# Kernel tuning notes

Measured on AMD Instinct MI355X. Metric: run time of the kernel, lower is better.

## Reference

```python
import jax, jax.numpy as jnp
import numpy as np

B, N, C, H = 32, 577, 768, 12
D = C // H  # head_dim = 64


def _rotate_half(t):
    half = t.shape[-1] // 2
    return jnp.concatenate([-t[..., half:], t[..., :half]], axis=-1)


def _rope(t, sin, cos):
    # t: [B, H, N-1, D]; sin/cos: [N-1, D] broadcast over batch and heads
    return t * cos + _rotate_half(t) * sin


def setup_inputs() -> dict:
    key = jax.random.key(0)
    ks = jax.random.split(key, 5)
    x = jax.random.normal(ks[0], (B, N, C), dtype=jnp.float32)
    w_qkv = jax.random.normal(ks[1], (C, 3 * C), dtype=jnp.float32) * (1.0 / np.sqrt(C))
    b_qkv = jnp.zeros((3 * C,), dtype=jnp.float32)
    w_proj = jax.random.normal(ks[2], (C, C), dtype=jnp.float32) * (1.0 / np.sqrt(C))
    b_proj = jnp.zeros((C,), dtype=jnp.float32)
    # rotary tables for the N-1 non-CLS tokens
    pos = jnp.arange(N - 1, dtype=jnp.float32)[:, None]            # [N-1, 1]
    inv_freq = 1.0 / (10000.0 ** (jnp.arange(0, D, 2, dtype=jnp.float32) / D))  # [D/2]
    ang = pos * inv_freq[None, :]                                   # [N-1, D/2]
    ang = jnp.concatenate([ang, ang], axis=-1)                      # [N-1, D]
    rope_sin = jnp.sin(ang)
    rope_cos = jnp.cos(ang)
    return {"x": x, "w_qkv": w_qkv, "b_qkv": b_qkv, "w_proj": w_proj,
            "b_proj": b_proj, "rope_sin": rope_sin, "rope_cos": rope_cos}


def reference(x, w_qkv, b_qkv, w_proj, b_proj, rope_sin, rope_cos):
    Bx, Nx, Cx = x.shape
    qkv = x @ w_qkv + b_qkv                                   # [B, N, 3C]
    qkv = qkv.reshape(Bx, Nx, 3, H, D).transpose(2, 0, 3, 1, 4)  # [3, B, H, N, D]
    q, k, v = qkv[0], qkv[1], qkv[2]
    # RoPE only on non-CLS tokens (index 0 is CLS)
    q = jnp.concatenate([q[:, :, :1, :], _rope(q[:, :, 1:, :], rope_sin, rope_cos)], axis=2)
    k = jnp.concatenate([k[:, :, :1, :], _rope(k[:, :, 1:, :], rope_sin, rope_cos)], axis=2)
    q = q / jnp.sqrt(jnp.float32(D))
    attn = jnp.einsum("bhqd,bhkd->bhqk", q, k)               # [B, H, N, N]
    attn = jax.nn.softmax(attn.astype(jnp.float32), axis=-1).astype(x.dtype)
    out = jnp.einsum("bhqk,bhkd->bhqd", attn, v)             # [B, H, N, D]
    out = out.transpose(0, 2, 1, 3).reshape(Bx, Nx, Cx)       # [B, N, C]
    return out @ w_proj + b_proj
```

## Files before the change

kernel.cpp:

```cpp
#include <hip/hip_runtime.h>

#define Bdim 32
#define Ndim 577
#define Cdim 768
#define Hdim 12
#define Ddim 64
#define Mdim (Bdim*Ndim)
#define VSTRIDE 640
#define TSTRIDE 152
#define QSCALE 0.18033688f
#define MGRP 19

typedef __attribute__((ext_vector_type(4))) float f32x4;
typedef __attribute__((ext_vector_type(8))) __bf16 bf16x8;
typedef __attribute__((ext_vector_type(4))) __bf16 bf16x4;

__device__ __forceinline__ void gl_lds16(const __bf16* g, __bf16* l) {
  __builtin_amdgcn_global_load_lds((const __attribute__((address_space(1))) void*)g,
                                   (__attribute__((address_space(3))) void*)l, 16, 0, 0);
}

__global__ __launch_bounds__(256) void f32_to_bf16(const float4* __restrict__ in,
                                                   bf16x4* __restrict__ out, int n4) {
  int i = blockIdx.x * 256 + threadIdx.x;
  if (i < n4) {
    float4 v = in[i];
    bf16x4 o = {(__bf16)v.x, (__bf16)v.y, (__bf16)v.z, (__bf16)v.w};
    out[i] = o;
  }
}

__global__ __launch_bounds__(256) void transpose_f32_bf16(const float* __restrict__ in,
                                                          __bf16* __restrict__ out,
                                                          int R, int Cc) {
  __shared__ float tile[64][65];
  int bx = blockIdx.x * 64;
  int by = blockIdx.y * 64;
  int tx = threadIdx.x & 63, ty = threadIdx.x >> 6;
  for (int i = ty; i < 64; i += 4) {
    int r = by + i, c = bx + tx;
    tile[i][tx] = (r < R && c < Cc) ? in[(size_t)r * Cc + c] : 0.f;
  }
  __syncthreads();
  for (int i = ty; i < 64; i += 4) {
    int r = bx + i, c = by + tx;
    if (r < Cc && c < R) out[(size_t)r * R + c] = (__bf16)tile[tx][i];
  }
}

__global__ __launch_bounds__(256) void transpose_f32_wfrag(const float* __restrict__ in,
                                                           __bf16* __restrict__ out) {
  __shared__ float tile[64][65];
  int bx = blockIdx.x * 64;
  int by = blockIdx.y * 64;
  int tx = threadIdx.x & 63, ty = threadIdx.x >> 6;
  #pragma unroll
  for (int i = ty; i < 64; i += 4)
    tile[i][tx] = in[(size_t)(by + i) * 2304 + bx + tx];
  __syncthreads();
  #pragma unroll
  for (int it = 0; it < 2; ++it) {
    int idx = it * 256 + threadIdx.x;
    int nl = idx & 63, kc = idx >> 6;
    bf16x8 o;
    #pragma unroll
    for (int j = 0; j < 8; ++j) o[j] = (__bf16)tile[kc * 8 + j][nl];
    int n = bx + nl, kk = by + kc * 8;
    *(bf16x8*)(out + ((size_t)(n >> 4) * 96 + (kk >> 3)) * 128 + (n & 15) * 8) = o;
  }
}

__device__ __forceinline__ void gemm_split_core(const __bf16* __restrict__ A,
                                                const __bf16* __restrict__ WF,
                                                int m0, int n0,
                                                __bf16* As, f32x4 acc[4][4]) {
  const int t = threadIdx.x;
  const int lane = t & 63, w = t >> 6;
  const int quad = lane >> 4, l16 = lane & 15;
  const int wm = w >> 1, wn = w & 1;
  const int nb16 = (n0 >> 4) + wn * 4;

  for (int k0 = 0; k0 < 768; k0 += 64) {
    __syncthreads();
    bf16x8 b[2][4];
    #pragma unroll
    for (int s = 0; s < 2; ++s)
      #pragma unroll
      for (int i = 0; i < 4; ++i)
        b[s][i] = *(const bf16x8*)(WF +
            ((size_t)(nb16 + i) * 96 + (k0 >> 3) + s * 4 + quad) * 128 + l16 * 8);
    #pragma unroll
    for (int e = 0; e < 4; ++e) {
      int h = e >> 1;
      int j = ((e & 1) << 2) | w;
      int row = j * 16 + (lane >> 2);
      int col = k0 + h * 32 + (lane & 3) * 8;
      int ar = m0 + row; if (ar > Mdim - 1) ar = Mdim - 1;
      gl_lds16(A + (size_t)ar * 768 + col, As + h * 4096 + j * 512 + lane * 8);
    }
    __syncthreads();
    #pragma unroll
    for (int s = 0; s < 2; ++s) {
      bf16x8 a[4];
      #pragma unroll
      for (int i = 0; i < 4; ++i)
        a[i] = *(const bf16x8*)(As + s * 4096 + (wm * 64 + i * 16 + l16) * 32 + quad * 8);
      #pragma unroll
      for (int mt = 0; mt < 4; ++mt)
        #pragma unroll
        for (int nt = 0; nt < 4; ++nt)
          acc[mt][nt] = __builtin_amdgcn_mfma_f32_16x16x32_bf16(a[mt], b[s][nt], acc[mt][nt], 0, 0, 0);
    }
  }
}

__device__ __forceinline__ void gemm_bt_core(const __bf16* __restrict__ A,
                                             const __bf16* __restrict__ BT,
                                             int m0, int n0,
                                             __bf16* As, __bf16* Bs,
                                             f32x4 acc[4][4]) {
  const int t = threadIdx.x;
  const int lane = t & 63, w = t >> 6;
  const int quad = lane >> 4, l16 = lane & 15;
  const int wm = w >> 1, wn = w & 1;

  for (int k0 = 0; k0 < 768; k0 += 64) {
    __syncthreads();
    #pragma unroll
    for (int e = 0; e < 4; ++e) {
      int h = e >> 1;
      int j = ((e & 1) << 2) | w;
      int row = j * 16 + (lane >> 2);
      int col = k0 + h * 32 + (lane & 3) * 8;
      int ar = m0 + row; if (ar > Mdim - 1) ar = Mdim - 1;
      __bf16* dstA = As + h * 4096 + j * 512 + lane * 8;
      __bf16* dstB = Bs + h * 4096 + j * 512 + lane * 8;
      gl_lds16(A  + (size_t)ar * 768 + col, dstA);
      gl_lds16(BT + (size_t)(n0 + row) * 768 + col, dstB);
    }
    __syncthreads();
    #pragma unroll
    for (int s = 0; s < 2; ++s) {
      bf16x8 a[4], b[4];
      #pragma unroll
      for (int i = 0; i < 4; ++i) {
        a[i] = *(const bf16x8*)(As + s * 4096 + (wm * 64 + i * 16 + l16) * 32 + quad * 8);
        b[i] = *(const bf16x8*)(Bs + s * 4096 + (wn * 64 + i * 16 + l16) * 32 + quad * 8);
      }
      #pragma unroll
      for (int mt = 0; mt < 4; ++mt)
        #pragma unroll
        for (int nt = 0; nt < 4; ++nt)
          acc[mt][nt] = __builtin_amdgcn_mfma_f32_16x16x32_bf16(a[mt], b[nt], acc[mt][nt], 0, 0, 0);
    }
  }
}

__device__ __forceinline__ bool xcd_decode(int lin, int nb, int mb, int& n, int& m) {
  int x8 = lin & 7;
  int rest = lin >> 3;
  n = rest % nb;
  int mg = rest / nb;
  m = mg * 8 + x8;
  return m < mb;
}

__global__ __launch_bounds__(256) void qk_kernel(const __bf16* __restrict__ x,
                                                 const __bf16* __restrict__ wf,
                                                 const float* __restrict__ b_qkv,
                                                 const float* __restrict__ rs,
                                                 const float* __restrict__ rc,
                                                 __bf16* __restrict__ q,
                                                 __bf16* __restrict__ k) {
  __shared__ __bf16 As[2 * 128 * 32];
  int nb, mbk;
  if (!xcd_decode(blockIdx.x, 12, 145, nb, mbk)) return;
  const int n0 = nb * 128, m0 = mbk * 128;

  f32x4 acc[4][4];
  const f32x4 fz = {0.f, 0.f, 0.f, 0.f};
  for (int i = 0; i < 4; ++i) for (int j = 0; j < 4; ++j) acc[i][j] = fz;
  gemm_split_core(x, wf, m0, n0, As, acc);

  const int lane = threadIdx.x & 63, w = threadIdx.x >> 6;
  const int quad = lane >> 4, l16 = lane & 15;
  const int wm = w >> 1, wn = w & 1;
  const int colbase = n0 + wn * 64;
  const int matrix = colbase / 768;
  const int head = (colbase % 768) / 64;

  #pragma unroll
  for (int mt = 0; mt < 4; ++mt) {
    int mbase = m0 + wm * 64 + mt * 16 + quad * 4;
    #pragma unroll
    for (int r = 0; r < 4; ++r) {
      int m = mbase + r;
      if (m >= Mdim) continue;
      int bb = m / 577, tok = m % 577;
      #pragma unroll
      for (int nt = 0; nt < 4; ++nt) {
        int d = nt * 16 + l16;
        float val = acc[mt][nt][r] + b_qkv[colbase + d];
        if (tok > 0) {
          float partner = acc[mt][nt ^ 2][r] + b_qkv[colbase + (d ^ 32)];
          float sn = rs[(size_t)(tok - 1) * 64 + d];
          float cs = rc[(size_t)(tok - 1) * 64 + d];
          float rot = (d < 32) ? -partner : partner;
          val = val * cs + rot * sn;
        }
        __bf16* dst;
        if (matrix == 0) { val *= QSCALE; dst = q; } else dst = k;
        dst[((size_t)(bb * 12 + head) * 577 + tok) * 64 + d] = (__bf16)val;
      }
    }
  }
}

__global__ __launch_bounds__(256) void v_kernel(const __bf16* __restrict__ x,
                                                const __bf16* __restrict__ wf,
                                                const float* __restrict__ b_qkv,
                                                __bf16* __restrict__ vt) {
  __shared__ __bf16 As[2 * 128 * 32];
  __shared__ __bf16 Ts[64 * TSTRIDE];
  int nb, mbk;
  if (!xcd_decode(blockIdx.x, 6, 145, nb, mbk)) return;
  const int n0 = 1536 + nb * 128, m0 = mbk * 128;

  f32x4 acc[4][4];
  const f32x4 fz = {0.f, 0.f, 0.f, 0.f};
  for (int i = 0; i < 4; ++i) for (int j = 0; j < 4; ++j) acc[i][j] = fz;
  gemm_split_core(x, wf, m0, n0, As, acc);

  const int t = threadIdx.x;
  const int lane = t & 63, w = t >> 6;
  const int quad = lane >> 4, l16 = lane & 15;
  const int wm = w >> 1, wn = w & 1;
  const int colbase = n0 + wn * 64;

  #pragma unroll
  for (int h = 0; h < 2; ++h) {
    __syncthreads();
    if (wn == h) {
      #pragma unroll
      for (int mt = 0; mt < 4; ++mt) {
        int tokbase = wm * 64 + mt * 16 + quad * 4;
        #pragma unroll
        for (int r = 0; r < 4; ++r) {
          #pragma unroll
          for (int nt = 0; nt < 4; ++nt) {
            int dl = nt * 16 + l16;
            Ts[dl * TSTRIDE + tokbase + r] =
                (__bf16)(acc[mt][nt][r] + b_qkv[colbase + dl]);
          }
        }
      }
    }
    __syncthreads();
    int hh = (n0 + h * 64 - 1536) / 64;
    #pragma unroll
    for (int it = 0; it < 4; ++it) {
      int c = it * 256 + t;
      int dl = c >> 4, chunk = c & 15;
      bf16x8 vv = *(const bf16x8*)(Ts + dl * TSTRIDE + chunk * 8);
      #pragma unroll
      for (int j = 0; j < 8; ++j) {
        int m = m0 + chunk * 8 + j;
        if (m < Mdim) {
          int bb = m / 577, tok = m % 577;
          vt[((size_t)(bb * 12 + hh) * 64 + dl) * VSTRIDE + tok] = vv[j];
        }
      }
    }
  }
}

__global__ __launch_bounds__(256) void attn_kernel(const __bf16* __restrict__ q,
                                                   const __bf16* __restrict__ k,
                                                   const __bf16* __restrict__ vt,
                                                   __bf16* __restrict__ ao) {
  __shared__ __bf16 qs[4096];
  __shared__ __bf16 ks[4096];
  __shared__ __bf16 vs[4096];
  __shared__ __bf16 ps[64 * 72];

  const int x8 = blockIdx.x & 7;
  const int rest = blockIdx.x >> 3;
  const int qt = rest % 10;
  const int bh = (rest / 10) * 8 + x8;

  const int t = threadIdx.x;
  const int lane = t & 63, w = t >> 6;
  const int quad = lane >> 4, l16 = lane & 15;

  const __bf16* qbase = q + (size_t)bh * 577 * 64;
  const __bf16* kbase = k + (size_t)bh * 577 * 64;
  const __bf16* vbase = vt + (size_t)bh * 64 * VSTRIDE;

  #pragma unroll
  for (int p = 0; p < 2; ++p) {
    int g = p * 256 + t;
    int d8 = g >> 6, tok = g & 63;
    gl_lds16(qbase + (size_t)(qt * 64 + tok) * 64 + d8 * 8, qs + (size_t)g * 8);
  }

  bf16x8 kreg[2], vreg[2];
  #pragma unroll
  for (int p = 0; p < 2; ++p) {
    int g = p * 256 + t;
    kreg[p] = *(const bf16x8*)(kbase + (size_t)(g & 63) * 64 + (g >> 6) * 8);
    vreg[p] = *(const bf16x8*)(vbase + (size_t)(g & 63) * VSTRIDE + (g >> 6) * 8);
  }

  f32x4 O[4]; const f32x4 fz = {0.f, 0.f, 0.f, 0.f};
  for (int i = 0; i < 4; ++i) O[i] = fz;
  float l_part[4] = {0.f, 0.f, 0.f, 0.f};

  for (int kt = 0; kt < 10; ++kt) {
    __syncthreads();
    #pragma unroll
    for (int p = 0; p < 2; ++p) {
      int g = p * 256 + t;
      *(bf16x8*)(ks + (size_t)g * 8) = kreg[p];
      *(bf16x8*)(vs + (size_t)g * 8) = vreg[p];
    }
    __syncthreads();

    if (kt < 9) {
      #pragma unroll
      for (int p = 0; p < 2; ++p) {
        int g = p * 256 + t;
        kreg[p] = *(const bf16x8*)(kbase + (size_t)((kt + 1) * 64 + (g & 63)) * 64 + (g >> 6) * 8);
        vreg[p] = *(const bf16x8*)(vbase + (size_t)(g & 63) * VSTRIDE + (kt + 1) * 64 + (g >> 6) * 8);
      }
      __builtin_amdgcn_sched_barrier(0);
    }

    f32x4 S[4]; for (int i = 0; i < 4; ++i) S[i] = fz;
    __builtin_amdgcn_s_setprio(1);
    #pragma unroll
    for (int step = 0; step < 2; ++step) {
      bf16x8 a = *(const bf16x8*)(qs + (size_t)((step * 4 + quad) * 64 + w * 16 + l16) * 8);
      #pragma unroll
      for (int nt = 0; nt < 4; ++nt) {
        bf16x8 b = *(const bf16x8*)(ks + (size_t)((step * 4 + quad) * 64 + nt * 16 + l16) * 8);
        S[nt] = __builtin_amdgcn_mfma_f32_16x16x32_bf16(a, b, S[nt], 0, 0, 0);
      }
    }
    __builtin_amdgcn_s_setprio(0);

    int kv_left = 577 - kt * 64;
    if (kv_left < 64) {
      #pragma unroll
      for (int nt = 0; nt < 4; ++nt) {
        int c = nt * 16 + l16;
        if (c >= kv_left) { S[nt][0] = -1e30f; S[nt][1] = -1e30f; S[nt][2] = -1e30f; S[nt][3] = -1e30f; }
      }
    }

    #pragma unroll
    for (int r = 0; r < 4; ++r) {
      #pragma unroll
      for (int nt = 0; nt < 4; ++nt) {
        float e = exp2f(S[nt][r]);
        l_part[r] += e;
        ps[(size_t)(w * 16 + quad * 4 + r) * 72 + nt * 16 + l16] = (__bf16)e;
      }
    }

    __builtin_amdgcn_s_setprio(1);
    #pragma unroll
    for (int step = 0; step < 2; ++step) {
      bf16x8 a = *(const bf16x8*)(ps + (size_t)(w * 16 + l16) * 72 + step * 32 + quad * 8);
      #pragma unroll
      for (int dt = 0; dt < 4; ++dt) {
        bf16x8 b = *(const bf16x8*)(vs + (size_t)((step * 4 + quad) * 64 + dt * 16 + l16) * 8);
        O[dt] = __builtin_amdgcn_mfma_f32_16x16x32_bf16(a, b, O[dt], 0, 0, 0);
      }
    }
    __builtin_amdgcn_s_setprio(0);
  }

  const int bb = bh / 12, hh = bh % 12;
  const int qrow0 = qt * 64 + w * 16 + quad * 4;
  #pragma unroll
  for (int r = 0; r < 4; ++r) {
    float l = l_part[r];
    l += __shfl_xor(l, 1); l += __shfl_xor(l, 2);
    l += __shfl_xor(l, 4); l += __shfl_xor(l, 8);
    int row = qrow0 + r;
    if (row < 577) {
      float inv = 1.f / l;
      size_t base = ((size_t)(bb * 577 + row)) * 768 + hh * 64;
      #pragma unroll
      for (int dt = 0; dt < 4; ++dt)
        ao[base + dt * 16 + l16] = (__bf16)(O[dt][r] * inv);
    }
  }
}

__global__ __launch_bounds__(256) void proj_kernel(const __bf16* __restrict__ ao,
                                                   const __bf16* __restrict__ wprojT,
                                                   const float* __restrict__ b_proj,
                                                   float* __restrict__ out) {
  __shared__ __bf16 As[2 * 128 * 32];
  __shared__ __bf16 Bs[2 * 128 * 32];
  int nb, mbk;
  if (!xcd_decode(blockIdx.x, 6, 145, nb, mbk)) return;
  const int n0 = nb * 128, m0 = mbk * 128;

  f32x4 acc[4][4];
  const f32x4 fz = {0.f, 0.f, 0.f, 0.f};
  for (int i = 0; i < 4; ++i) for (int j = 0; j < 4; ++j) acc[i][j] = fz;
  gemm_bt_core(ao, wprojT, m0, n0, As, Bs, acc);

  const int lane = threadIdx.x & 63, w = threadIdx.x >> 6;
  const int quad = lane >> 4, l16 = lane & 15;
  const int wm = w >> 1, wn = w & 1;
  const int colbase = n0 + wn * 64;

  #pragma unroll
  for (int mt = 0; mt < 4; ++mt) {
    int mbase = m0 + wm * 64 + mt * 16 + quad * 4;
    #pragma unroll
    for (int r = 0; r < 4; ++r) {
      int m = mbase + r;
      if (m >= Mdim) continue;
      #pragma unroll
      for (int nt = 0; nt < 4; ++nt) {
        int c = colbase + nt * 16 + l16;
        out[(size_t)m * 768 + c] = acc[mt][nt][r] + b_proj[c];
      }
    }
  }
}

extern "C" void kernel_launch(void* const* d_in, const int* in_sizes, int n_in,
                              void* d_out, int out_size, void* d_ws, size_t ws_size,
                              hipStream_t stream) {
  const float* x      = (const float*)d_in[0];
  const float* w_qkv  = (const float*)d_in[1];
  const float* b_qkv  = (const float*)d_in[2];
  const float* w_proj = (const float*)d_in[3];
  const float* b_proj = (const float*)d_in[4];
  const float* rsn    = (const float*)d_in[5];
  const float* rcs    = (const float*)d_in[6];
  float* out = (float*)d_out;

  constexpr size_t QK_E = (size_t)Bdim * Hdim * Ndim * Ddim;
  constexpr size_t VT_E = (size_t)Bdim * Hdim * Ddim * VSTRIDE;
  constexpr size_t AO_E = (size_t)Mdim * Cdim;
  __bf16* q      = (__bf16*)d_ws;
  __bf16* k      = q + QK_E;
  __bf16* vt     = k + QK_E;
  __bf16* ao     = vt + VT_E;
  __bf16* xb     = ao;
  __bf16* wqkvF  = ao + AO_E;
  __bf16* wprojT = wqkvF + (size_t)2304 * 768;

  f32_to_bf16<<<13848, 256, 0, stream>>>((const float4*)x, (bf16x4*)xb,
                                         (int)(AO_E / 4));
  transpose_f32_wfrag<<<dim3(36, 12), 256, 0, stream>>>(w_qkv, wqkvF);
  transpose_f32_bf16<<<dim3(12, 12), 256, 0, stream>>>(w_proj, wprojT, 768, 768);
  qk_kernel<<<8 * MGRP * 12, 256, 0, stream>>>(xb, wqkvF, b_qkv, rsn, rcs, q, k);
  v_kernel<<<8 * MGRP * 6, 256, 0, stream>>>(xb, wqkvF, b_qkv, vt);
  attn_kernel<<<3840, 256, 0, stream>>>(q, k, vt, ao);
  proj_kernel<<<8 * MGRP * 6, 256, 0, stream>>>(ao, wprojT, b_proj, out);
}
```

Measured before the change: 432.3 us.

## Register-prefetch A tiles in split GEMM core and reuse it for projection

The split GEMM core stops using direct global-to-LDS loads for the A tile. It now prefetches the next k-slice of A into registers during the MFMA loop and stores it to LDS at the start of the next iteration, so global latency overlaps compute. The projection GEMM now uses the same fragment-packed weight layout and core, with B fragments read straight from global memory, which removes its B shared-memory tile. The cost is more registers per thread and an extra register-to-LDS store step.

```diff
diff --git a/kernel.cpp b/kernel.cpp
--- a/kernel.cpp
+++ b/kernel.cpp
@@ -30,33 +30,16 @@
   }
 }
 
-__global__ __launch_bounds__(256) void transpose_f32_bf16(const float* __restrict__ in,
-                                                          __bf16* __restrict__ out,
-                                                          int R, int Cc) {
+__global__ __launch_bounds__(256) void transpose_f32_wfrag(const float* __restrict__ in,
+                                                           __bf16* __restrict__ out,
+                                                           int Cc) {
   __shared__ float tile[64][65];
   int bx = blockIdx.x * 64;
   int by = blockIdx.y * 64;
   int tx = threadIdx.x & 63, ty = threadIdx.x >> 6;
-  for (int i = ty; i < 64; i += 4) {
-    int r = by + i, c = bx + tx;
-    tile[i][tx] = (r < R && c < Cc) ? in[(size_t)r * Cc + c] : 0.f;
-  }
-  __syncthreads();
-  for (int i = ty; i < 64; i += 4) {
-    int r = bx + i, c = by + tx;
-    if (r < Cc && c < R) out[(size_t)r * R + c] = (__bf16)tile[tx][i];
-  }
-}
-
-__global__ __launch_bounds__(256) void transpose_f32_wfrag(const float* __restrict__ in,
-                                                           __bf16* __restrict__ out) {
-  __shared__ float tile[64][65];
-  int bx = blockIdx.x * 64;
-  int by = blockIdx.y * 64;
-  int tx = threadIdx.x & 63, ty = threadIdx.x >> 6;
   #pragma unroll
   for (int i = ty; i < 64; i += 4)
-    tile[i][tx] = in[(size_t)(by + i) * 2304 + bx + tx];
+    tile[i][tx] = in[(size_t)(by + i) * Cc + bx + tx];
   __syncthreads();
   #pragma unroll
   for (int it = 0; it < 2; ++it) {
@@ -80,8 +63,28 @@
   const int wm = w >> 1, wn = w & 1;
   const int nb16 = (n0 >> 4) + wn * 4;
 
+  int arow_g[4]; int acol_g[4]; int adst[4];
+  #pragma unroll
+  for (int e = 0; e < 4; ++e) {
+    int h = e >> 1;
+    int j = ((e & 1) << 2) | w;
+    int row = j * 16 + (lane >> 2);
+    int ar = m0 + row; if (ar > Mdim - 1) ar = Mdim - 1;
+    arow_g[e] = ar;
+    acol_g[e] = h * 32 + (lane & 3) * 8;
+    adst[e] = h * 4096 + j * 512 + lane * 8;
+  }
+
+  bf16x8 areg[4];
+  #pragma unroll
+  for (int e = 0; e < 4; ++e)
+    areg[e] = *(const bf16x8*)(A + (size_t)arow_g[e] * 768 + acol_g[e]);
+
   for (int k0 = 0; k0 < 768; k0 += 64) {
     __syncthreads();
+    #pragma unroll
+    for (int e = 0; e < 4; ++e)
+      *(bf16x8*)(As + adst[e]) = areg[e];
     bf16x8 b[2][4];
     #pragma unroll
     for (int s = 0; s < 2; ++s)
@@ -89,16 +92,15 @@
       for (int i = 0; i < 4; ++i)
         b[s][i] = *(const bf16x8*)(WF +
             ((size_t)(nb16 + i) * 96 + (k0 >> 3) + s * 4 + quad) * 128 + l16 * 8);
-    #pragma unroll
-    for (int e = 0; e < 4; ++e) {
-      int h = e >> 1;
-      int j = ((e & 1) << 2) | w;
-      int row = j * 16 + (lane >> 2);
-      int col = k0 + h * 32 + (lane & 3) * 8;
-      int ar = m0 + row; if (ar > Mdim - 1) ar = Mdim - 1;
-      gl_lds16(A + (size_t)ar * 768 + col, As + h * 4096 + j * 512 + lane * 8);
-    }
-    __syncthreads();
+    __syncthreads();
+
+    if (k0 < 704) {
+      #pragma unroll
+      for (int e = 0; e < 4; ++e)
+        areg[e] = *(const bf16x8*)(A + (size_t)arow_g[e] * 768 + (k0 + 64) + acol_g[e]);
+      __builtin_amdgcn_sched_barrier(0);
+    }
+
     #pragma unroll
     for (int s = 0; s < 2; ++s) {
       bf16x8 a[4];
@@ -110,48 +112,6 @@
         #pragma unroll
         for (int nt = 0; nt < 4; ++nt)
           acc[mt][nt] = __builtin_amdgcn_mfma_f32_16x16x32_bf16(a[mt], b[s][nt], acc[mt][nt], 0, 0, 0);
-    }
-  }
-}
-
-__device__ __forceinline__ void gemm_bt_core(const __bf16* __restrict__ A,
-                                             const __bf16* __restrict__ BT,
-                                             int m0, int n0,
-                                             __bf16* As, __bf16* Bs,
-                                             f32x4 acc[4][4]) {
-  const int t = threadIdx.x;
-  const int lane = t & 63, w = t >> 6;
-  const int quad = lane >> 4, l16 = lane & 15;
-  const int wm = w >> 1, wn = w & 1;
-
-  for (int k0 = 0; k0 < 768; k0 += 64) {
-    __syncthreads();
-    #pragma unroll
-    for (int e = 0; e < 4; ++e) {
-      int h = e >> 1;
-      int j = ((e & 1) << 2) | w;
-      int row = j * 16 + (lane >> 2);
-      int col = k0 + h * 32 + (lane & 3) * 8;
-      int ar = m0 + row; if (ar > Mdim - 1) ar = Mdim - 1;
-      __bf16* dstA = As + h * 4096 + j * 512 + lane * 8;
-      __bf16* dstB = Bs + h * 4096 + j * 512 + lane * 8;
-      gl_lds16(A  + (size_t)ar * 768 + col, dstA);
-      gl_lds16(BT + (size_t)(n0 + row) * 768 + col, dstB);
-    }
-    __syncthreads();
-    #pragma unroll
-    for (int s = 0; s < 2; ++s) {
-      bf16x8 a[4], b[4];
-      #pragma unroll
-      for (int i = 0; i < 4; ++i) {
-        a[i] = *(const bf16x8*)(As + s * 4096 + (wm * 64 + i * 16 + l16) * 32 + quad * 8);
-        b[i] = *(const bf16x8*)(Bs + s * 4096 + (wn * 64 + i * 16 + l16) * 32 + quad * 8);
-      }
-      #pragma unroll
-      for (int mt = 0; mt < 4; ++mt)
-        #pragma unroll
-        for (int nt = 0; nt < 4; ++nt)
-          acc[mt][nt] = __builtin_amdgcn_mfma_f32_16x16x32_bf16(a[mt], b[nt], acc[mt][nt], 0, 0, 0);
     }
   }
 }
@@ -399,11 +359,10 @@
 }
 
 __global__ __launch_bounds__(256) void proj_kernel(const __bf16* __restrict__ ao,
-                                                   const __bf16* __restrict__ wprojT,
+                                                   const __bf16* __restrict__ wprojF,
                                                    const float* __restrict__ b_proj,
                                                    float* __restrict__ out) {
   __shared__ __bf16 As[2 * 128 * 32];
-  __shared__ __bf16 Bs[2 * 128 * 32];
   int nb, mbk;
   if (!xcd_decode(blockIdx.x, 6, 145, nb, mbk)) return;
   const int n0 = nb * 128, m0 = mbk * 128;
@@ -411,7 +370,7 @@
   f32x4 acc[4][4];
   const f32x4 fz = {0.f, 0.f, 0.f, 0.f};
   for (int i = 0; i < 4; ++i) for (int j = 0; j < 4; ++j) acc[i][j] = fz;
-  gemm_bt_core(ao, wprojT, m0, n0, As, Bs, acc);
+  gemm_split_core(ao, wprojF, m0, n0, As, acc);
 
   const int lane = threadIdx.x & 63, w = threadIdx.x >> 6;
   const int quad = lane >> 4, l16 = lane & 15;
@@ -455,14 +414,14 @@
   __bf16* ao     = vt + VT_E;
   __bf16* xb     = ao;
   __bf16* wqkvF  = ao + AO_E;
-  __bf16* wprojT = wqkvF + (size_t)2304 * 768;
+  __bf16* wprojF = wqkvF + (size_t)2304 * 768;
 
   f32_to_bf16<<<13848, 256, 0, stream>>>((const float4*)x, (bf16x4*)xb,
                                          (int)(AO_E / 4));
-  transpose_f32_wfrag<<<dim3(36, 12), 256, 0, stream>>>(w_qkv, wqkvF);
-  transpose_f32_bf16<<<dim3(12, 12), 256, 0, stream>>>(w_proj, wprojT, 768, 768);
+  transpose_f32_wfrag<<<dim3(36, 12), 256, 0, stream>>>(w_qkv, wqkvF, 2304);
+  transpose_f32_wfrag<<<dim3(12, 12), 256, 0, stream>>>(w_proj, wprojF, 768);
   qk_kernel<<<8 * MGRP * 12, 256, 0, stream>>>(xb, wqkvF, b_qkv, rsn, rcs, q, k);
   v_kernel<<<8 * MGRP * 6, 256, 0, stream>>>(xb, wqkvF, b_qkv, vt);
   attn_kernel<<<3840, 256, 0, stream>>>(q, k, vt, ao);
-  proj_kernel<<<8 * MGRP * 6, 256, 0, stream>>>(ao, wprojT, b_proj, out);
-}
+  proj_kernel<<<8 * MGRP * 6, 256, 0, stream>>>(ao, wprojF, b_proj, out);
+}
```

Result: no change. 434.3 us (+0.5%).
